# Optimization experiments

Measured on AMD Instinct MI355X. Metric: run time of the kernel, lower is better.

Reference implementation:

```python
import jax, jax.numpy as jnp
import numpy as np

N, E = 50000, 800000
IN_DIM, HID, L, H = 128, 128, 3, 4
C = HID // H  # per-head channels
NEG_SLOPE = 0.2


def layer_norm(x, g, b, eps=1e-5):
    mu = jnp.mean(x, axis=-1, keepdims=True)
    var = jnp.var(x, axis=-1, keepdims=True)
    return (x - mu) * jax.lax.rsqrt(var + eps) * g + b


def gatv2_conv(x, edge_index, Wl, bl, Wr, br, att, conv_b):
    # x: [N, HID]; edge_index: [2, E]; Wl/Wr: [HID, HID]; att: [H, C]
    src, dst = edge_index[0], edge_index[1]
    xl = (x @ Wl + bl).reshape(N, H, C)  # source transform
    xr = (x @ Wr + br).reshape(N, H, C)  # target transform
    e = jax.nn.leaky_relu(xl[src] + xr[dst], NEG_SLOPE)      # [E, H, C]
    alpha = jnp.einsum('ehc,hc->eh', e, att)                  # [E, H]
    # segment softmax over incoming edges of each dst node
    amax = jax.ops.segment_max(alpha, dst, num_segments=N)    # [N, H]
    ex = jnp.exp(alpha - amax[dst])
    denom = jax.ops.segment_sum(ex, dst, num_segments=N)[dst] + 1e-16
    w = ex / denom                                            # [E, H]
    out = jax.ops.segment_sum(xl[src] * w[:, :, None], dst, num_segments=N)
    return out.reshape(N, HID) + conv_b


def setup_inputs() -> dict:
    key = jax.random.key(0)
    ks = jax.random.split(key, 24)
    s = 0.05
    inp = {
        'x': jax.random.normal(ks[0], (N, IN_DIM), jnp.float32),
        'edge_index': jax.random.randint(ks[1], (2, E), 0, N, jnp.int64),
        'Win': jax.random.normal(ks[2], (IN_DIM, HID)) * s,
        'b_in': jnp.zeros((HID,)),
        'ln_g': jnp.ones((L, HID)),
        'ln_b': jnp.zeros((L, HID)),
        'Wl': jax.random.normal(ks[3], (L, HID, HID)) * s,
        'bl': jnp.zeros((L, HID)),
        'Wr': jax.random.normal(ks[4], (L, HID, HID)) * s,
        'br': jnp.zeros((L, HID)),
        'att': jax.random.normal(ks[5], (L, H, C)) * s,
        'conv_b': jnp.zeros((L, HID)),
        'fn_g': jnp.ones((HID,)),
        'fn_b': jnp.zeros((HID,)),
        'pW1': jax.random.normal(ks[6], (HID, HID // 2)) * s,
        'pb1': jnp.zeros((HID // 2,)),
        'pW2': jax.random.normal(ks[7], (HID // 2, 1)) * s,
        'pb2': jnp.zeros((1,)),
        'vW1': jax.random.normal(ks[8], (HID, HID // 2)) * s,
        'vb1': jnp.zeros((HID // 2,)),
        'vW2': jax.random.normal(ks[9], (HID // 2, HID)) * s,
        'vb2': jnp.zeros((HID,)),
    }
    return inp


def reference(x, edge_index, Win, b_in, ln_g, ln_b, Wl, bl, Wr, br, att, conv_b,
              fn_g, fn_b, pW1, pb1, pW2, pb2, vW1, vb1, vW2, vb2):
    h = x @ Win + b_in  # input_proj
    # GNNResidualBlock (assumed pre-norm residual): h = h + gelu(conv(LN(h)))
    for i in range(L):
        z = layer_norm(h, ln_g[i], ln_b[i])
        z = gatv2_conv(z, edge_index, Wl[i], bl[i], Wr[i], br[i], att[i], conv_b[i])
        h = h + jax.nn.gelu(z)
    h = layer_norm(h, fn_g, fn_b)
    prob_logits = jax.nn.gelu(h @ pW1 + pb1) @ pW2 + pb2   # [N, 1]
    volume_emb = jax.nn.gelu(h @ vW1 + vb1) @ vW2 + vb2     # [N, HID]
    return (volume_emb, prob_logits)
```

## Files before the change

kernel.cpp:

```cpp
#include <hip/hip_runtime.h>
#include <math.h>

constexpr int NN  = 50000;
constexpr int EE  = 800000;
constexpr int NPAD = 50176;
constexpr float LOG2E = 1.4426950408889634f;

typedef short bf16x8 __attribute__((ext_vector_type(8)));
typedef float f32x4  __attribute__((ext_vector_type(4)));

__device__ __forceinline__ unsigned f2bfu(float f) {
    union { float f; unsigned u; } x; x.f = f;
    unsigned r = x.u + 0x7fffu + ((x.u >> 16) & 1u);
    return r >> 16;
}
__device__ __forceinline__ short f2bf(float f) { return (short)f2bfu(f); }
__device__ __forceinline__ unsigned pack2(float lo, float hi) {
    return f2bfu(lo) | (f2bfu(hi) << 16);
}
__device__ __forceinline__ float bfbits_lo(unsigned w) { return __uint_as_float(w << 16); }
__device__ __forceinline__ float bfbits_hi(unsigned w) { return __uint_as_float(w & 0xffff0000u); }

__device__ __forceinline__ float gelu_tanh(float x) {
    float u = 0.7978845608028654f * (x + 0.044715f * x * x * x);
    float t = 1.0f - 2.0f / (__expf(2.0f * u) + 1.0f);
    return 0.5f * x * (1.0f + t);
}

__device__ __forceinline__ float dpp_add16(float x) {
    int t;
    t = __builtin_amdgcn_update_dpp(0, __float_as_int(x), 0xB1,  0xf, 0xf, true);
    x += __int_as_float(t);
    t = __builtin_amdgcn_update_dpp(0, __float_as_int(x), 0x4E,  0xf, 0xf, true);
    x += __int_as_float(t);
    t = __builtin_amdgcn_update_dpp(0, __float_as_int(x), 0x141, 0xf, 0xf, true);
    x += __int_as_float(t);
    t = __builtin_amdgcn_update_dpp(0, __float_as_int(x), 0x140, 0xf, 0xf, true);
    x += __int_as_float(t);
    return x;
}

struct WtArgs {
    const float* src[10];
    short*       dst[10];
    int K[10];
    int N[10];
};

template<int BN, int NB, int DO_LN, int ACT, int OUTBF0, int OUTBF1>
__device__ __forceinline__ void ln_gemm_body(
    int row0, const float* __restrict__ A,
    const float* __restrict__ lg, const float* __restrict__ lb,
    const short* __restrict__ B0t, const float* __restrict__ bias0, void* __restrict__ C0,
    const short* __restrict__ B1t, const float* __restrict__ bias1, void* __restrict__ C1,
    int nrows, short* As, short* Bs)
{
    constexpr int K = 128, KP = 136;
    constexpr int NF = BN / 16;
    constexpr int CH = K / 8;
    const int tid = threadIdx.x;

    {
        int r = tid >> 2, q = tid & 3;
        int grow = row0 + r;
        bool ok = grow < nrows;
        float4 v[8];
        const float* src = A + (size_t)grow * K + q * 32;
#pragma unroll
        for (int i = 0; i < 8; ++i)
            v[i] = ok ? *reinterpret_cast<const float4*>(src + i * 4)
                      : make_float4(0.f, 0.f, 0.f, 0.f);
        if (DO_LN) {
            float s = 0.f, s2 = 0.f;
#pragma unroll
            for (int i = 0; i < 8; ++i) {
                s  += v[i].x + v[i].y + v[i].z + v[i].w;
                s2 += v[i].x * v[i].x + v[i].y * v[i].y + v[i].z * v[i].z + v[i].w * v[i].w;
            }
            s += __shfl_xor(s, 1); s2 += __shfl_xor(s2, 1);
            s += __shfl_xor(s, 2); s2 += __shfl_xor(s2, 2);
            float mean = s * (1.f / 128.f);
            float var  = s2 * (1.f / 128.f) - mean * mean;
            float rstd = rsqrtf(var + 1e-5f);
#pragma unroll
            for (int i = 0; i < 8; ++i) {
                float4 gg = *reinterpret_cast<const float4*>(lg + q * 32 + i * 4);
                float4 bb = *reinterpret_cast<const float4*>(lb + q * 32 + i * 4);
                v[i].x = (v[i].x - mean) * rstd * gg.x + bb.x;
                v[i].y = (v[i].y - mean) * rstd * gg.y + bb.y;
                v[i].z = (v[i].z - mean) * rstd * gg.z + bb.z;
                v[i].w = (v[i].w - mean) * rstd * gg.w + bb.w;
            }
        }
        short* dst = &As[r * KP + q * 32];
#pragma unroll
        for (int i = 0; i < 4; ++i) {
            uint4 w = make_uint4(pack2(v[2*i].x,   v[2*i].y),
                                 pack2(v[2*i].z,   v[2*i].w),
                                 pack2(v[2*i+1].x, v[2*i+1].y),
                                 pack2(v[2*i+1].z, v[2*i+1].w));
            *reinterpret_cast<uint4*>(dst + i * 8) = w;
        }
    }

    auto stageB = [&](const short* __restrict__ Bt) {
#pragma unroll
        for (int it = 0; it < BN * CH / 256; ++it) {
            int idx = tid + it * 256;
            int nn = idx / CH, j = idx % CH;
            *reinterpret_cast<uint4*>(&Bs[nn * KP + j * 8]) =
                *reinterpret_cast<const uint4*>(&Bt[nn * K + j * 8]);
        }
    };
    stageB(B0t);
    __syncthreads();

    const int wave = tid >> 6;
    const int lane = tid & 63;
    const int kg   = lane >> 4;
    const int lr   = lane & 15;

    bf16x8 afrag[4];
#pragma unroll
    for (int kk = 0; kk < 4; ++kk)
        afrag[kk] = *reinterpret_cast<const bf16x8*>(
            &As[(wave * 16 + lr) * KP + kk * 32 + kg * 8]);

    auto do_gemm = [&](const float* __restrict__ bias, void* __restrict__ Cv, bool outbf) {
        f32x4 acc[NF];
#pragma unroll
        for (int nf = 0; nf < NF; ++nf) acc[nf] = (f32x4){0.f, 0.f, 0.f, 0.f};
#pragma unroll
        for (int nf = 0; nf < NF; ++nf) {
#pragma unroll
            for (int kk = 0; kk < 4; ++kk) {
                bf16x8 bfrag = *reinterpret_cast<const bf16x8*>(
                    &Bs[(nf * 16 + lr) * KP + kk * 32 + kg * 8]);
                acc[nf] = __builtin_amdgcn_mfma_f32_16x16x32_bf16(
                    afrag[kk], bfrag, acc[nf], 0, 0, 0);
            }
        }
#pragma unroll
        for (int nf = 0; nf < NF; ++nf) {
            int col = nf * 16 + lr;
            float bi = bias[col];
#pragma unroll
            for (int j = 0; j < 4; ++j) {
                int row = row0 + wave * 16 + kg * 4 + j;
                if (row < nrows) {
                    float v = acc[nf][j] + bi;
                    if (ACT == 1) v = gelu_tanh(v);
                    if (outbf) ((short*)Cv)[(size_t)row * BN + col] = f2bf(v);
                    else       ((float*)Cv)[(size_t)row * BN + col] = v;
                }
            }
        }
    };

    do_gemm(bias0, C0, OUTBF0 != 0);
    if (NB == 2) {
        __syncthreads();
        stageB(B1t);
        __syncthreads();
        do_gemm(bias1, C1, OUTBF1 != 0);
    }
}

__global__ __launch_bounds__(256) void hybrid1(
    const int* __restrict__ ei, int* __restrict__ counts, int* __restrict__ pos, WtArgs a)
{
    if (blockIdx.x < 1024) {
        for (int e = blockIdx.x * 256 + threadIdx.x; e < EE; e += 1024 * 256)
            pos[e] = atomicAdd(&counts[ei[EE + e]], 1);
    } else {
        int bb = blockIdx.x - 1024;
        int m = bb >> 4, slice = bb & 15;
        const float* s = a.src[m];
        short* d = a.dst[m];
        int K = a.K[m], N = a.N[m], total = K * N;
        for (int i = slice * 256 + threadIdx.x; i < total; i += 16 * 256) {
            int k = i / N, n = i - k * N;
            d[n * K + k] = f2bf(s[i]);
        }
    }
}

__device__ void scan256(const int* __restrict__ counts, int* __restrict__ roff) {
    __shared__ int wsum[4];
    __shared__ int tilesum;
    int tid = threadIdx.x, wid = tid >> 6, lane = tid & 63;
    int carry = 0;
    for (int base = 0; base < NPAD; base += 1024) {
        int idx = base + tid * 4;
        int4 c = *reinterpret_cast<const int4*>(&counts[idx]);
        int s0 = c.x, s1 = s0 + c.y, s2 = s1 + c.z, s3 = s2 + c.w;
        int x = s3;
#pragma unroll
        for (int off = 1; off < 64; off <<= 1) {
            int t = __shfl_up(x, off);
            if (lane >= off) x += t;
        }
        if (lane == 63) wsum[wid] = x;
        __syncthreads();
        if (tid == 0) {
            int a0 = wsum[0], a1 = wsum[1], a2 = wsum[2], a3 = wsum[3];
            wsum[0] = 0; wsum[1] = a0; wsum[2] = a0 + a1; wsum[3] = a0 + a1 + a2;
            tilesum = a0 + a1 + a2 + a3;
        }
        __syncthreads();
        int start = carry + wsum[wid] + (x - s3);
        int4 o = make_int4(start, start + s0, start + s1, start + s2);
        *reinterpret_cast<int4*>(&roff[idx]) = o;
        carry += tilesum;
        __syncthreads();
    }
}

__global__ __launch_bounds__(256) void hybrid2(
    const int* __restrict__ counts, int* __restrict__ roff,
    const float* __restrict__ x, const short* __restrict__ Win_t,
    const float* __restrict__ b_in, float* __restrict__ h, int nrows)
{
    __shared__ short As[64 * 136];
    __shared__ short Bs[128 * 136];
    if (blockIdx.x == 0) {
        scan256(counts, roff);
    } else {
        ln_gemm_body<128, 1, 0, 0, 0, 0>((blockIdx.x - 1) * 64, x, nullptr,
            nullptr, Win_t, b_in, h, nullptr, nullptr, nullptr, nrows, As, Bs);
    }
}

__global__ __launch_bounds__(256) void hybrid3(
    const int* __restrict__ ei, const int* __restrict__ roff,
    const int* __restrict__ pos, int* __restrict__ ssrc,
    const float* __restrict__ h, const float* __restrict__ lg, const float* __restrict__ lb,
    const short* __restrict__ Wl_t, const float* __restrict__ bl, short* __restrict__ XL,
    const short* __restrict__ Wr_t, const float* __restrict__ br, short* __restrict__ XR,
    int nrows)
{
    __shared__ short As[64 * 136];
    __shared__ short Bs[128 * 136];
    if (blockIdx.x < 512) {
        for (int e = blockIdx.x * 256 + threadIdx.x; e < EE; e += 512 * 256)
            ssrc[roff[ei[EE + e]] + pos[e]] = ei[e] << 8;
    } else {
        ln_gemm_body<128, 2, 1, 0, 1, 1>((blockIdx.x - 512) * 64, h,
            lg, lb, Wl_t, bl, XL, Wr_t, br, XR, nrows, As, Bs);
    }
}

__global__ __launch_bounds__(256) void fused_layer(
    const float* __restrict__ h, const float* __restrict__ lg, const float* __restrict__ lb,
    const short* __restrict__ Wl_t, const float* __restrict__ bl, short* __restrict__ XL,
    const short* __restrict__ Wr_t, const float* __restrict__ br, short* __restrict__ XR,
    int nrows)
{
    __shared__ short As[64 * 136];
    __shared__ short Bs[128 * 136];
    ln_gemm_body<128, 2, 1, 0, 1, 1>(blockIdx.x * 64, h, lg, lb,
        Wl_t, bl, XL, Wr_t, br, XR, nrows, As, Bs);
}

__global__ __launch_bounds__(256) void gat_node_kernel(
    const short* __restrict__ XL, const short* __restrict__ XR,
    const int* __restrict__ roff, const int* __restrict__ ssrc,
    const float* __restrict__ att, const float* __restrict__ conv_b,
    float* __restrict__ h)
{
    int n = blockIdx.x * 4 + (threadIdx.x >> 6);
    if (n >= NN) return;
    int lane = threadIdx.x & 63;
    int j0 = lane * 2;
    unsigned wr = *reinterpret_cast<const unsigned*>(&XR[(size_t)n * 128 + j0]);
    float xr0 = bfbits_lo(wr), xr1 = bfbits_hi(wr);
    float2 at = *reinterpret_cast<const float2*>(&att[j0]);
    float a6x = at.x * (0.6f * LOG2E), a4x = at.x * (0.4f * LOG2E);
    float a6y = at.y * (0.6f * LOG2E), a4y = at.y * (0.4f * LOG2E);

    float dA = 0.f, a0A = 0.f, a1A = 0.f;
    float dB = 0.f, a0B = 0.f, a1B = 0.f;

    const char* XLb = (const char*)XL;
    const unsigned lbyte = (unsigned)lane * 4u;

    auto proc = [&](unsigned w, float& d, float& a0, float& a1) {
        float x0 = bfbits_lo(w), x1 = bfbits_hi(w);
        float s0 = x0 + xr0;
        float s1 = x1 + xr1;
        float part = fmaf(s0, a6x,
                     fmaf(__builtin_fabsf(s0), a4x,
                     fmaf(s1, a6y, __builtin_fabsf(s1) * a4y)));
        part = dpp_add16(part);
        float pe = __builtin_amdgcn_exp2f(part);
        d += pe;
        a0 = fmaf(pe, x0, a0);
        a1 = fmaf(pe, x1, a1);
    };

    int beg = roff[n], end = roff[n + 1], p = beg;
    for (; p + 3 < end; p += 4) {
        unsigned o0 = (unsigned)ssrc[p]     + lbyte;
        unsigned o1 = (unsigned)ssrc[p + 1] + lbyte;
        unsigned o2 = (unsigned)ssrc[p + 2] + lbyte;
        unsigned o3 = (unsigned)ssrc[p + 3] + lbyte;
        unsigned w0 = *reinterpret_cast<const unsigned*>(XLb + o0);
        unsigned w1 = *reinterpret_cast<const unsigned*>(XLb + o1);
        unsigned w2 = *reinterpret_cast<const unsigned*>(XLb + o2);
        unsigned w3 = *reinterpret_cast<const unsigned*>(XLb + o3);
        proc(w0, dA, a0A, a1A);
        proc(w1, dB, a0B, a1B);
        proc(w2, dA, a0A, a1A);
        proc(w3, dB, a0B, a1B);
    }
    for (; p < end; ++p) {
        unsigned w0 = *reinterpret_cast<const unsigned*>(
            XLb + ((unsigned)ssrc[p] + lbyte));
        proc(w0, dA, a0A, a1A);
    }
    float d    = dA + dB;
    float acc0 = a0A + a0B;
    float acc1 = a1A + a1B;

    float inv = 1.f / (d + 1e-16f);
    float2 cb = *reinterpret_cast<const float2*>(&conv_b[j0]);
    float o0 = gelu_tanh(fmaf(acc0, inv, cb.x));
    float o1 = gelu_tanh(fmaf(acc1, inv, cb.y));
    float2 hv = *reinterpret_cast<const float2*>(&h[(size_t)n * 128 + j0]);
    hv.x += o0; hv.y += o1;
    *reinterpret_cast<float2*>(&h[(size_t)n * 128 + j0]) = hv;
}

__global__ __launch_bounds__(256) void final_head_full(
    const float* __restrict__ A,
    const float* __restrict__ lg, const float* __restrict__ lb,
    const short* __restrict__ pW1t, const float* __restrict__ pb1,
    const float* __restrict__ pW2, const float* __restrict__ pb2,
    const short* __restrict__ vW1t, const float* __restrict__ vb1,
    const short* __restrict__ vW2t, const float* __restrict__ vb2,
    float* __restrict__ vol, float* __restrict__ prob, int nrows)
{
    constexpr int K = 128, KP = 136, KP2 = 72;
    constexpr int CH = K / 8;
    __shared__ short As[64 * 136];
    __shared__ short Bs[128 * 136];

    const int tid  = threadIdx.x;
    const int row0 = blockIdx.x * 64;

    {
        int r = tid >> 2, q = tid & 3;
        int grow = row0 + r;
        bool ok = grow < nrows;
        float4 v[8];
        const float* src = A + (size_t)grow * K + q * 32;
#pragma unroll
        for (int i = 0; i < 8; ++i)
            v[i] = ok ? *reinterpret_cast<const float4*>(src + i * 4)
                      : make_float4(0.f, 0.f, 0.f, 0.f);
        float s = 0.f, s2 = 0.f;
#pragma unroll
        for (int i = 0; i < 8; ++i) {
            s  += v[i].x + v[i].y + v[i].z + v[i].w;
            s2 += v[i].x * v[i].x + v[i].y * v[i].y + v[i].z * v[i].z + v[i].w * v[i].w;
        }
        s += __shfl_xor(s, 1); s2 += __shfl_xor(s2, 1);
        s += __shfl_xor(s, 2); s2 += __shfl_xor(s2, 2);
        float mean = s * (1.f / 128.f);
        float var  = s2 * (1.f / 128.f) - mean * mean;
        float rstd = rsqrtf(var + 1e-5f);
        short* dst = &As[r * KP + q * 32];
#pragma unroll
        for (int i = 0; i < 8; ++i) {
            float4 gg = *reinterpret_cast<const float4*>(lg + q * 32 + i * 4);
            float4 bb = *reinterpret_cast<const float4*>(lb + q * 32 + i * 4);
            v[i].x = (v[i].x - mean) * rstd * gg.x + bb.x;
            v[i].y = (v[i].y - mean) * rstd * gg.y + bb.y;
            v[i].z = (v[i].z - mean) * rstd * gg.z + bb.z;
            v[i].w = (v[i].w - mean) * rstd * gg.w + bb.w;
        }
#pragma unroll
        for (int i = 0; i < 4; ++i) {
            uint4 w = make_uint4(pack2(v[2*i].x,   v[2*i].y),
                                 pack2(v[2*i].z,   v[2*i].w),
                                 pack2(v[2*i+1].x, v[2*i+1].y),
                                 pack2(v[2*i+1].z, v[2*i+1].w));
            *reinterpret_cast<uint4*>(dst + i * 8) = w;
        }
    }
#pragma unroll
    for (int it = 0; it < 8; ++it) {
        int idx = tid + it * 256;
        int nn = idx / CH, j = idx % CH;
        const short* srcw = (nn < 64) ? &pW1t[nn * K + j * 8]
                                      : &vW1t[(nn - 64) * K + j * 8];
        *reinterpret_cast<uint4*>(&Bs[nn * KP + j * 8]) =
            *reinterpret_cast<const uint4*>(srcw);
    }
    __syncthreads();

    const int wave = tid >> 6;
    const int lane = tid & 63;
    const int kg   = lane >> 4;
    const int lr   = lane & 15;

    bf16x8 afrag[4];
#pragma unroll
    for (int kk = 0; kk < 4; ++kk)
        afrag[kk] = *reinterpret_cast<const bf16x8*>(
            &As[(wave * 16 + lr) * KP + kk * 32 + kg * 8]);

    f32x4 acc_v[4];
#pragma unroll
    for (int nf = 0; nf < 4; ++nf) acc_v[nf] = (f32x4){0.f, 0.f, 0.f, 0.f};
#pragma unroll
    for (int nf = 0; nf < 4; ++nf)
#pragma unroll
        for (int kk = 0; kk < 4; ++kk) {
            bf16x8 bfrag = *reinterpret_cast<const bf16x8*>(
                &Bs[(64 + nf * 16 + lr) * KP + kk * 32 + kg * 8]);
            acc_v[nf] = __builtin_amdgcn_mfma_f32_16x16x32_bf16(
                afrag[kk], bfrag, acc_v[nf], 0, 0, 0);
        }

    {
        f32x4 acc[4];
#pragma unroll
        for (int nf = 0; nf < 4; ++nf) acc[nf] = (f32x4){0.f, 0.f, 0.f, 0.f};
#pragma unroll
        for (int nf = 0; nf < 4; ++nf)
#pragma unroll
            for (int kk = 0; kk < 4; ++kk) {
                bf16x8 bfrag = *reinterpret_cast<const bf16x8*>(
                    &Bs[(nf * 16 + lr) * KP + kk * 32 + kg * 8]);
                acc[nf] = __builtin_amdgcn_mfma_f32_16x16x32_bf16(
                    afrag[kk], bfrag, acc[nf], 0, 0, 0);
            }
        float pr[4] = {0.f, 0.f, 0.f, 0.f};
#pragma unroll
        for (int nf = 0; nf < 4; ++nf) {
            int col = nf * 16 + lr;
            float bi = pb1[col];
            float w2 = pW2[col];
#pragma unroll
            for (int j = 0; j < 4; ++j)
                pr[j] = fmaf(gelu_tanh(acc[nf][j] + bi), w2, pr[j]);
        }
#pragma unroll
        for (int j = 0; j < 4; ++j) {
            float v = dpp_add16(pr[j]);
            int row = row0 + wave * 16 + kg * 4 + j;
            if (lr == 0 && row < nrows) prob[row] = v + pb2[0];
        }
    }

    __syncthreads();
    short* t2lds = As;
#pragma unroll
    for (int nf = 0; nf < 4; ++nf) {
        int col = nf * 16 + lr;
        float bi = vb1[col];
#pragma unroll
        for (int j = 0; j < 4; ++j) {
            int r = wave * 16 + kg * 4 + j;
            t2lds[r * KP2 + col] = f2bf(gelu_tanh(acc_v[nf][j] + bi));
        }
    }
#pragma unroll
    for (int it = 0; it < 4; ++it) {
        int idx = tid + it * 256;
        int nn = idx >> 3, j = idx & 7;
        *reinterpret_cast<uint4*>(&Bs[nn * KP2 + j * 8]) =
            *reinterpret_cast<const uint4*>(&vW2t[nn * 64 + j * 8]);
    }
    __syncthreads();

    bf16x8 a2[2];
#pragma unroll
    for (int kk = 0; kk < 2; ++kk)
        a2[kk] = *reinterpret_cast<const bf16x8*>(
            &t2lds[(wave * 16 + lr) * KP2 + kk * 32 + kg * 8]);
    f32x4 accv[8];
#pragma unroll
    for (int nf = 0; nf < 8; ++nf) accv[nf] = (f32x4){0.f, 0.f, 0.f, 0.f};
#pragma unroll
    for (int nf = 0; nf < 8; ++nf)
#pragma unroll
        for (int kk = 0; kk < 2; ++kk) {
            bf16x8 bfrag = *reinterpret_cast<const bf16x8*>(
                &Bs[(nf * 16 + lr) * KP2 + kk * 32 + kg * 8]);
            accv[nf] = __builtin_amdgcn_mfma_f32_16x16x32_bf16(
                a2[kk], bfrag, accv[nf], 0, 0, 0);
        }
#pragma unroll
    for (int nf = 0; nf < 8; ++nf) {
        int col = nf * 16 + lr;
        float bi = vb2[col];
#pragma unroll
        for (int j = 0; j < 4; ++j) {
            int row = row0 + wave * 16 + kg * 4 + j;
            if (row < nrows)
                vol[(size_t)row * 128 + col] = accv[nf][j] + bi;
        }
    }
}

extern "C" void kernel_launch(void* const* d_in, const int* in_sizes, int n_in,
                              void* d_out, int out_size, void* d_ws, size_t ws_size,
                              hipStream_t stream)
{
    const float* x      = (const float*)d_in[0];
    const int*   ei     = (const int*)  d_in[1];
    const float* Win    = (const float*)d_in[2];
    const float* b_in   = (const float*)d_in[3];
    const float* ln_g   = (const float*)d_in[4];
    const float* ln_b   = (const float*)d_in[5];
    const float* Wl     = (const float*)d_in[6];
    const float* bl     = (const float*)d_in[7];
    const float* Wr     = (const float*)d_in[8];
    const float* br     = (const float*)d_in[9];
    const float* att    = (const float*)d_in[10];
    const float* conv_b = (const float*)d_in[11];
    const float* fn_g   = (const float*)d_in[12];
    const float* fn_b   = (const float*)d_in[13];
    const float* pW1    = (const float*)d_in[14];
    const float* pb1    = (const float*)d_in[15];
    const float* pW2    = (const float*)d_in[16];
    const float* pb2    = (const float*)d_in[17];
    const float* vW1    = (const float*)d_in[18];
    const float* vb1    = (const float*)d_in[19];
    const float* vW2    = (const float*)d_in[20];
    const float* vb2    = (const float*)d_in[21];

    char* wp = (char*)d_ws;
    float* h    = (float*)wp; wp += (size_t)NN * 128 * 4;
    short* XL   = (short*)wp; wp += (size_t)NN * 128 * 2;
    short* XR   = (short*)wp; wp += (size_t)NN * 128 * 2;
    int* counts = (int*)wp;   wp += (size_t)NPAD * 4;
    int* roff   = (int*)wp;   wp += (size_t)(NPAD + 16) * 4;
    int* pos    = (int*)wp;   wp += (size_t)EE * 4;
    int* ssrc   = (int*)wp;   wp += (size_t)EE * 4;
    short* Win_t = (short*)wp;
    short* Wl_t  = Win_t + 16384;
    short* Wr_t  = Wl_t + 3 * 16384;
    short* pW1_t = Wr_t + 3 * 16384;
    short* vW1_t = pW1_t + 8192;
    short* vW2_t = vW1_t + 8192;
    float* vol  = (float*)d_out;
    float* prob = (float*)d_out + (size_t)NN * 128;

    WtArgs wa;
    wa.src[0] = Win;  wa.dst[0] = Win_t; wa.K[0] = 128; wa.N[0] = 128;
    for (int i = 0; i < 3; ++i) {
        wa.src[1 + i] = Wl + (size_t)i * 16384; wa.dst[1 + i] = Wl_t + i * 16384;
        wa.K[1 + i] = 128; wa.N[1 + i] = 128;
        wa.src[4 + i] = Wr + (size_t)i * 16384; wa.dst[4 + i] = Wr_t + i * 16384;
        wa.K[4 + i] = 128; wa.N[4 + i] = 128;
    }
    wa.src[7] = pW1; wa.dst[7] = pW1_t; wa.K[7] = 128; wa.N[7] = 64;
    wa.src[8] = vW1; wa.dst[8] = vW1_t; wa.K[8] = 128; wa.N[8] = 64;
    wa.src[9] = vW2; wa.dst[9] = vW2_t; wa.K[9] = 64;  wa.N[9] = 128;

    const int gemm_grid = (NN + 63) / 64;
    const int row_grid  = (NN + 3) / 4;

    hipMemsetAsync(counts, 0, (size_t)NPAD * sizeof(int), stream);
    hybrid1<<<1024 + 160, 256, 0, stream>>>(ei, counts, pos, wa);
    hybrid2<<<1 + gemm_grid, 256, 0, stream>>>(counts, roff, x, Win_t, b_in, h, NN);
    hybrid3<<<512 + gemm_grid, 256, 0, stream>>>(ei, roff, pos, ssrc,
        h, ln_g, ln_b, Wl_t, bl, XL, Wr_t, br, XR, NN);
    gat_node_kernel<<<row_grid, 256, 0, stream>>>(
        XL, XR, roff, ssrc, att, conv_b, h);
    for (int i = 1; i < 3; ++i) {
        fused_layer<<<gemm_grid, 256, 0, stream>>>(
            h, ln_g + i * 128, ln_b + i * 128,
            Wl_t + i * 16384, bl + i * 128, XL,
            Wr_t + i * 16384, br + i * 128, XR, NN);
        gat_node_kernel<<<row_grid, 256, 0, stream>>>(
            XL, XR, roff, ssrc, att + i * 128, conv_b + i * 128, h);
    }
    final_head_full<<<gemm_grid, 256, 0, stream>>>(
        h, fn_g, fn_b, pW1_t, pb1, pW2, pb2, vW1_t, vb1, vW2_t, vb2, vol, prob, NN);
}
```

Before: 374.5 us.

## Scatter CSR edges by XCC-local destination ranges with dynamic work claiming

```diff
diff --git a/kernel.cpp b/kernel.cpp
--- a/kernel.cpp
+++ b/kernel.cpp
@@ -5,6 +5,10 @@
 constexpr int EE  = 800000;
 constexpr int NPAD = 50176;
 constexpr float LOG2E = 1.4426950408889634f;
+constexpr int NRANGE = 8;
+constexpr int NCHUNK = 64;
+constexpr int RSPAN  = NPAD / NRANGE;
+constexpr int ESPAN  = EE / NCHUNK;
 
 typedef short bf16x8 __attribute__((ext_vector_type(8)));
 typedef float f32x4  __attribute__((ext_vector_type(4)));
@@ -25,6 +29,12 @@
     float u = 0.7978845608028654f * (x + 0.044715f * x * x * x);
     float t = 1.0f - 2.0f / (__expf(2.0f * u) + 1.0f);
     return 0.5f * x * (1.0f + t);
+}
+
+__device__ __forceinline__ int get_xcc() {
+    int x;
+    asm volatile("s_getreg_b32 %0, hwreg(HW_REG_XCC_ID)" : "=s"(x));
+    return x & 7;
 }
 
 __device__ __forceinline__ float dpp_add16(float x) {
@@ -167,11 +177,11 @@
 }
 
 __global__ __launch_bounds__(256) void hybrid1(
-    const int* __restrict__ ei, int* __restrict__ counts, int* __restrict__ pos, WtArgs a)
+    const int* __restrict__ ei, int* __restrict__ counts, WtArgs a)
 {
     if (blockIdx.x < 1024) {
         for (int e = blockIdx.x * 256 + threadIdx.x; e < EE; e += 1024 * 256)
-            pos[e] = atomicAdd(&counts[ei[EE + e]], 1);
+            atomicAdd(&counts[ei[EE + e]], 1);
     } else {
         int bb = blockIdx.x - 1024;
         int m = bb >> 4, slice = bb & 15;
@@ -233,7 +243,7 @@
 
 __global__ __launch_bounds__(256) void hybrid3(
     const int* __restrict__ ei, const int* __restrict__ roff,
-    const int* __restrict__ pos, int* __restrict__ ssrc,
+    int* __restrict__ cur, int* __restrict__ ssrc, int* __restrict__ misc,
     const float* __restrict__ h, const float* __restrict__ lg, const float* __restrict__ lb,
     const short* __restrict__ Wl_t, const float* __restrict__ bl, short* __restrict__ XL,
     const short* __restrict__ Wr_t, const float* __restrict__ br, short* __restrict__ XR,
@@ -242,8 +252,66 @@
     __shared__ short As[64 * 136];
     __shared__ short Bs[128 * 136];
     if (blockIdx.x < 512) {
-        for (int e = blockIdx.x * 256 + threadIdx.x; e < EE; e += 512 * 256)
-            ssrc[roff[ei[EE + e]] + pos[e]] = ei[e] << 8;
+        int* nextq    = misc;
+        int* claimed  = misc + 8;
+        int* claimcnt = misc + 8 + 512;
+        const int tid = threadIdx.x;
+        __shared__ int s_w;
+
+        auto process = [&](int w) {
+            int r = w >> 6, c = w & 63;
+            int lo = r * RSPAN, hi = lo + RSPAN;
+            int e1 = c * ESPAN + ESPAN;
+            for (int e = c * ESPAN + tid; e < e1; e += 256) {
+                int d = ei[EE + e];
+                if (d >= lo && d < hi) {
+                    int p = atomicAdd(&cur[d], 1);
+                    ssrc[roff[d] + p] = ei[e] << 8;
+                }
+            }
+        };
+
+        const int xcc = get_xcc();
+        while (true) {
+            if (tid == 0) {
+                int t = atomicAdd(&nextq[xcc], 1);
+                int w = -1;
+                if (t < NCHUNK) {
+                    int cand = xcc * NCHUNK + t;
+                    if (atomicExch(&claimed[cand], 1) == 0) {
+                        atomicAdd(claimcnt, 1);
+                        w = cand;
+                    } else w = -2;
+                }
+                s_w = w;
+            }
+            __syncthreads();
+            int w = s_w;
+            __syncthreads();
+            if (w == -1) break;
+            if (w >= 0) process(w);
+        }
+        while (true) {
+            if (tid == 0) {
+                int w = -1;
+                if (*(volatile int*)claimcnt < 512) {
+                    for (int i = 0; i < 512; ++i) {
+                        if (((volatile int*)claimed)[i] == 0 &&
+                            atomicExch(&claimed[i], 1) == 0) {
+                            atomicAdd(claimcnt, 1);
+                            w = i;
+                            break;
+                        }
+                    }
+                }
+                s_w = w;
+            }
+            __syncthreads();
+            int w = s_w;
+            __syncthreads();
+            if (w < 0) break;
+            process(w);
+        }
     } else {
         ln_gemm_body<128, 2, 1, 0, 1, 1>((blockIdx.x - 512) * 64, h,
             lg, lb, Wl_t, bl, XL, Wr_t, br, XR, nrows, As, Bs);
@@ -537,8 +605,9 @@
     short* XL   = (short*)wp; wp += (size_t)NN * 128 * 2;
     short* XR   = (short*)wp; wp += (size_t)NN * 128 * 2;
     int* counts = (int*)wp;   wp += (size_t)NPAD * 4;
+    int* cur    = (int*)wp;   wp += (size_t)NPAD * 4;
+    int* misc   = (int*)wp;   wp += (size_t)1024 * 4;
     int* roff   = (int*)wp;   wp += (size_t)(NPAD + 16) * 4;
-    int* pos    = (int*)wp;   wp += (size_t)EE * 4;
     int* ssrc   = (int*)wp;   wp += (size_t)EE * 4;
     short* Win_t = (short*)wp;
     short* Wl_t  = Win_t + 16384;
@@ -564,10 +633,10 @@
     const int gemm_grid = (NN + 63) / 64;
     const int row_grid  = (NN + 3) / 4;
 
-    hipMemsetAsync(counts, 0, (size_t)NPAD * sizeof(int), stream);
-    hybrid1<<<1024 + 160, 256, 0, stream>>>(ei, counts, pos, wa);
+    hipMemsetAsync(counts, 0, ((size_t)2 * NPAD + 1024) * sizeof(int), stream);
+    hybrid1<<<1024 + 160, 256, 0, stream>>>(ei, counts, wa);
     hybrid2<<<1 + gemm_grid, 256, 0, stream>>>(counts, roff, x, Win_t, b_in, h, NN);
-    hybrid3<<<512 + gemm_grid, 256, 0, stream>>>(ei, roff, pos, ssrc,
+    hybrid3<<<512 + gemm_grid, 256, 0, stream>>>(ei, roff, cur, ssrc, misc,
         h, ln_g, ln_b, Wl_t, bl, XL, Wr_t, br, XR, NN);
     gat_node_kernel<<<row_grid, 256, 0, stream>>>(
         XL, XR, roff, ssrc, att, conv_b, h);
```

Result: slower. 410.6 us (+9.6%).

## Process two edges per wavefront with 4 channels per lane in GAT node kernel

Applied to the files above, without the earlier changes.

```diff
diff --git a/kernel.cpp b/kernel.cpp
--- a/kernel.cpp
+++ b/kernel.cpp
@@ -36,6 +36,17 @@
     t = __builtin_amdgcn_update_dpp(0, __float_as_int(x), 0x141, 0xf, 0xf, true);
     x += __int_as_float(t);
     t = __builtin_amdgcn_update_dpp(0, __float_as_int(x), 0x140, 0xf, 0xf, true);
+    x += __int_as_float(t);
+    return x;
+}
+
+__device__ __forceinline__ float dpp_add8(float x) {
+    int t;
+    t = __builtin_amdgcn_update_dpp(0, __float_as_int(x), 0xB1,  0xf, 0xf, true);
+    x += __int_as_float(t);
+    t = __builtin_amdgcn_update_dpp(0, __float_as_int(x), 0x4E,  0xf, 0xf, true);
+    x += __int_as_float(t);
+    t = __builtin_amdgcn_update_dpp(0, __float_as_int(x), 0x141, 0xf, 0xf, true);
     x += __int_as_float(t);
     return x;
 }
@@ -270,65 +281,89 @@
 {
     int n = blockIdx.x * 4 + (threadIdx.x >> 6);
     if (n >= NN) return;
-    int lane = threadIdx.x & 63;
-    int j0 = lane * 2;
-    unsigned wr = *reinterpret_cast<const unsigned*>(&XR[(size_t)n * 128 + j0]);
-    float xr0 = bfbits_lo(wr), xr1 = bfbits_hi(wr);
-    float2 at = *reinterpret_cast<const float2*>(&att[j0]);
-    float a6x = at.x * (0.6f * LOG2E), a4x = at.x * (0.4f * LOG2E);
-    float a6y = at.y * (0.6f * LOG2E), a4y = at.y * (0.4f * LOG2E);
-
-    float dA = 0.f, a0A = 0.f, a1A = 0.f;
-    float dB = 0.f, a0B = 0.f, a1B = 0.f;
+    const int lane = threadIdx.x & 63;
+    const int half = lane >> 5;
+    const int pos  = lane & 31;
+
+    uint2 wr2 = *reinterpret_cast<const uint2*>(&XR[(size_t)n * 128 + pos * 4]);
+    const float xr0 = bfbits_lo(wr2.x), xr1 = bfbits_hi(wr2.x);
+    const float xr2 = bfbits_lo(wr2.y), xr3 = bfbits_hi(wr2.y);
+    float4 at = *reinterpret_cast<const float4*>(&att[pos * 4]);
+    const float a6_0 = at.x * (0.6f * LOG2E), a4_0 = at.x * (0.4f * LOG2E);
+    const float a6_1 = at.y * (0.6f * LOG2E), a4_1 = at.y * (0.4f * LOG2E);
+    const float a6_2 = at.z * (0.6f * LOG2E), a4_2 = at.z * (0.4f * LOG2E);
+    const float a6_3 = at.w * (0.6f * LOG2E), a4_3 = at.w * (0.4f * LOG2E);
+
+    float dA = 0.f, dB = 0.f;
+    float aA0 = 0.f, aA1 = 0.f, aA2 = 0.f, aA3 = 0.f;
+    float aB0 = 0.f, aB1 = 0.f, aB2 = 0.f, aB3 = 0.f;
 
     const char* XLb = (const char*)XL;
-    const unsigned lbyte = (unsigned)lane * 4u;
-
-    auto proc = [&](unsigned w, float& d, float& a0, float& a1) {
-        float x0 = bfbits_lo(w), x1 = bfbits_hi(w);
-        float s0 = x0 + xr0;
-        float s1 = x1 + xr1;
-        float part = fmaf(s0, a6x,
-                     fmaf(__builtin_fabsf(s0), a4x,
-                     fmaf(s1, a6y, __builtin_fabsf(s1) * a4y)));
-        part = dpp_add16(part);
+    const unsigned lbyte = (unsigned)pos * 8u;
+
+    auto proc = [&](uint2 w, bool valid, float& d,
+                    float& a0, float& a1, float& a2, float& a3) {
+        float x0 = bfbits_lo(w.x), x1 = bfbits_hi(w.x);
+        float x2 = bfbits_lo(w.y), x3 = bfbits_hi(w.y);
+        float s0 = x0 + xr0, s1 = x1 + xr1, s2 = x2 + xr2, s3 = x3 + xr3;
+        float part =
+            fmaf(s0, a6_0, fmaf(__builtin_fabsf(s0), a4_0,
+            fmaf(s1, a6_1, fmaf(__builtin_fabsf(s1), a4_1,
+            fmaf(s2, a6_2, fmaf(__builtin_fabsf(s2), a4_2,
+            fmaf(s3, a6_3, __builtin_fabsf(s3) * a4_3)))))));
+        part = dpp_add8(part);
         float pe = __builtin_amdgcn_exp2f(part);
+        if (!valid) pe = 0.f;
         d += pe;
         a0 = fmaf(pe, x0, a0);
         a1 = fmaf(pe, x1, a1);
+        a2 = fmaf(pe, x2, a2);
+        a3 = fmaf(pe, x3, a3);
     };
 
-    int beg = roff[n], end = roff[n + 1], p = beg;
+    const int beg = roff[n], end = roff[n + 1];
+    int p = beg;
     for (; p + 3 < end; p += 4) {
-        unsigned o0 = (unsigned)ssrc[p]     + lbyte;
-        unsigned o1 = (unsigned)ssrc[p + 1] + lbyte;
-        unsigned o2 = (unsigned)ssrc[p + 2] + lbyte;
-        unsigned o3 = (unsigned)ssrc[p + 3] + lbyte;
-        unsigned w0 = *reinterpret_cast<const unsigned*>(XLb + o0);
-        unsigned w1 = *reinterpret_cast<const unsigned*>(XLb + o1);
-        unsigned w2 = *reinterpret_cast<const unsigned*>(XLb + o2);
-        unsigned w3 = *reinterpret_cast<const unsigned*>(XLb + o3);
-        proc(w0, dA, a0A, a1A);
-        proc(w1, dB, a0B, a1B);
-        proc(w2, dA, a0A, a1A);
-        proc(w3, dB, a0B, a1B);
-    }
-    for (; p < end; ++p) {
-        unsigned w0 = *reinterpret_cast<const unsigned*>(
-            XLb + ((unsigned)ssrc[p] + lbyte));
-        proc(w0, dA, a0A, a1A);
-    }
-    float d    = dA + dB;
-    float acc0 = a0A + a0B;
-    float acc1 = a1A + a1B;
-
-    float inv = 1.f / (d + 1e-16f);
-    float2 cb = *reinterpret_cast<const float2*>(&conv_b[j0]);
-    float o0 = gelu_tanh(fmaf(acc0, inv, cb.x));
-    float o1 = gelu_tanh(fmaf(acc1, inv, cb.y));
-    float2 hv = *reinterpret_cast<const float2*>(&h[(size_t)n * 128 + j0]);
-    hv.x += o0; hv.y += o1;
-    *reinterpret_cast<float2*>(&h[(size_t)n * 128 + j0]) = hv;
+        unsigned oA = (unsigned)ssrc[p + half]     + lbyte;
+        unsigned oB = (unsigned)ssrc[p + 2 + half] + lbyte;
+        uint2 wA = *reinterpret_cast<const uint2*>(XLb + oA);
+        uint2 wB = *reinterpret_cast<const uint2*>(XLb + oB);
+        proc(wA, true, dA, aA0, aA1, aA2, aA3);
+        proc(wB, true, dB, aB0, aB1, aB2, aB3);
+    }
+    if (p < end) {
+        int eA = p + half;
+        bool vA = eA < end;
+        unsigned oA = (unsigned)ssrc[vA ? eA : beg] + lbyte;
+        uint2 wA = *reinterpret_cast<const uint2*>(XLb + oA);
+        proc(wA, vA, dA, aA0, aA1, aA2, aA3);
+        if (p + 2 < end) {
+            int eB = p + 2 + half;
+            bool vB = eB < end;
+            unsigned oB = (unsigned)ssrc[vB ? eB : beg] + lbyte;
+            uint2 wB = *reinterpret_cast<const uint2*>(XLb + oB);
+            proc(wB, vB, dB, aB0, aB1, aB2, aB3);
+        }
+    }
+    float d  = dA + dB;
+    float c0 = aA0 + aB0, c1 = aA1 + aB1, c2 = aA2 + aB2, c3 = aA3 + aB3;
+    d  += __shfl_xor(d, 32);
+    c0 += __shfl_xor(c0, 32);
+    c1 += __shfl_xor(c1, 32);
+    c2 += __shfl_xor(c2, 32);
+    c3 += __shfl_xor(c3, 32);
+
+    if (half == 0) {
+        float inv = 1.f / (d + 1e-16f);
+        float* hp = &h[(size_t)n * 128 + pos * 4];
+        float4 hv = *reinterpret_cast<const float4*>(hp);
+        float4 cb = *reinterpret_cast<const float4*>(&conv_b[pos * 4]);
+        hv.x += gelu_tanh(fmaf(c0, inv, cb.x));
+        hv.y += gelu_tanh(fmaf(c1, inv, cb.y));
+        hv.z += gelu_tanh(fmaf(c2, inv, cb.z));
+        hv.w += gelu_tanh(fmaf(c3, inv, cb.w));
+        *reinterpret_cast<float4*>(hp) = hv;
+    }
 }
 
 __global__ __launch_bounds__(256) void final_head_full(
```

New measurement: 374.4 us. Within noise of the previous version (-0.0%).
